# Kernel optimization log

Measured on AMD Instinct MI355X. Metric: run time of the kernel, lower is better.

## Reference

```python
import jax, jax.numpy as jnp
import numpy as np

N_NODES = 100000
N_EDGES = 1600000
D = 128  # h_feats


def setup_inputs() -> dict:
    key = jax.random.key(0)
    k1, k2, k3, k4 = jax.random.split(key, 4)
    x = jax.random.normal(k1, (N_NODES, D), dtype=jnp.float32)
    edge_index = jax.random.randint(k2, (2, N_EDGES), 0, N_NODES, dtype=jnp.int64)
    # Linear(2D -> D), torch layout [out, in]
    W1 = jax.random.normal(k3, (D, 2 * D), dtype=jnp.float32) * (1.0 / np.sqrt(2 * D))
    b1 = jnp.zeros((D,), dtype=jnp.float32)
    # Linear(D -> 1)
    W2 = jax.random.normal(k4, (1, D), dtype=jnp.float32) * (1.0 / np.sqrt(D))
    b2 = jnp.zeros((1,), dtype=jnp.float32)
    return {"x": x, "edge_index": edge_index, "W1": W1, "b1": b1, "W2": W2, "b2": b2}


def reference(x, edge_index, W1, b1, W2, b2):
    # gather both endpoints and concat along features: [E, 2D]
    h = jnp.concatenate([x[edge_index[0]], x[edge_index[1]]], axis=-1)
    h = jax.nn.relu(h @ W1.T + b1)          # [E, D]
    h = h @ W2.T + b2                        # [E, 1]
    return h.squeeze(1)                      # [E]
```

## Files before the change

### kernel.cpp

```cpp
#include <hip/hip_runtime.h>
#include <hip/hip_bf16.h>

#define N_NODES 100000
#define N_EDGES 1600000
#define NT32    3125
#define PRE_BLKS 625

#define BQ_OFF 12800000
#define SA_OFF 25600000
#define SB_OFF 26000000

typedef __attribute__((ext_vector_type(8))) short short8v;
typedef __attribute__((ext_vector_type(4))) float float4v;

__device__ __forceinline__ unsigned short f2bf(float f) {
    unsigned int u = __float_as_uint(f);
    u += 0x7fffu + ((u >> 16) & 1u);
    return (unsigned short)(u >> 16);
}
__device__ __forceinline__ unsigned int pack2bf(float a, float b) {
    return (unsigned int)f2bf(a) | ((unsigned int)f2bf(b) << 16);
}
__device__ __forceinline__ float2 bfpair(unsigned int w) {
    return float2{__uint_as_float(w << 16), __uint_as_float(w & 0xffff0000u)};
}
#define MAGICB 12583040.0f
__device__ __forceinline__ unsigned int qmagic(float f, float inv) {
    return __float_as_uint(fmaf(f, inv, MAGICB));
}

__device__ __forceinline__ void quant_store(
    const unsigned short* __restrict__ xlds, unsigned char* __restrict__ Q,
    float* __restrict__ S, int n0, int tid) {
    const int row = tid >> 3, part = tid & 7;
    const unsigned short* src = xlds + row * 132 + part * 16;
    uint4 w0 = *reinterpret_cast<const uint4*>(src);
    uint4 w1 = *reinterpret_cast<const uint4*>(src + 8);
    unsigned int ws[8] = {w0.x, w0.y, w0.z, w0.w, w1.x, w1.y, w1.z, w1.w};
    float m = 1e-6f;
#pragma unroll
    for (int k = 0; k < 8; ++k) {
        float2 f = bfpair(ws[k]);
        m = fmaxf(m, fmaxf(fabsf(f.x), fabsf(f.y)));
    }
    m = fmaxf(m, __shfl_xor(m, 1));
    m = fmaxf(m, __shfl_xor(m, 2));
    m = fmaxf(m, __shfl_xor(m, 4));
    const float inv = 127.0f / m;
    unsigned int ob[4];
#pragma unroll
    for (int k = 0; k < 4; ++k) {
        float2 f0 = bfpair(ws[2 * k]);
        float2 f1 = bfpair(ws[2 * k + 1]);
        unsigned int q0 = qmagic(f0.x, inv), q1 = qmagic(f0.y, inv);
        unsigned int q2 = qmagic(f1.x, inv), q3 = qmagic(f1.y, inv);
        ob[k] = (q0 & 0xffu) | ((q1 & 0xffu) << 8) |
                ((q2 & 0xffu) << 16) | (q3 << 24);
    }
    const int n = n0 + row;
    *reinterpret_cast<uint4*>(Q + (size_t)n * 128 + part * 16) =
        uint4{ob[0], ob[1], ob[2], ob[3]};
    if (part == 0) S[n] = m * (1.0f / 127.0f);
}

__global__ __launch_bounds__(256) void precompute_kernel(
    const float* __restrict__ x, const float* __restrict__ W1,
    const float* __restrict__ b1, unsigned char* __restrict__ Aq,
    unsigned char* __restrict__ Bq, float* __restrict__ sA,
    float* __restrict__ sB) {
    __shared__ unsigned short wlds[256 * 132];
    __shared__ unsigned short xlds[32 * 132];

    const int tid = threadIdx.x;
    const int wave = tid >> 6, lane = tid & 63;
    const int quad = lane >> 4, l15 = lane & 15;

    float4 b1v[4];
    if (wave < 2) {
#pragma unroll
        for (int j = 0; j < 4; ++j)
            b1v[j] = *reinterpret_cast<const float4*>(b1 + wave * 64 + j * 16 + quad * 4);
    }

#pragma unroll
    for (int i = 0; i < 32; ++i) {
        int fi = tid + i * 256;
        int jc = fi >> 5, c4 = fi & 31;
        float4 w4 = reinterpret_cast<const float4*>(
            W1)[(size_t)(jc & 127) * 64 + (jc >> 7) * 32 + c4];
        unsigned int* d = reinterpret_cast<unsigned int*>(&wlds[jc * 132 + c4 * 4]);
        d[0] = pack2bf(w4.x, w4.y);
        d[1] = pack2bf(w4.z, w4.w);
    }

    float4 xr[4];
    int t = blockIdx.x;
#pragma unroll
    for (int i = 0; i < 4; ++i) {
        int fi = tid + i * 256;
        int n = fi >> 5, c4 = fi & 31;
        xr[i] = reinterpret_cast<const float4*>(x)[(size_t)(t * 32 + n) * 32 + c4];
    }

    for (; t < NT32; t += PRE_BLKS) {
        __syncthreads();
#pragma unroll
        for (int i = 0; i < 4; ++i) {
            int fi = tid + i * 256;
            int n = fi >> 5, c4 = fi & 31;
            unsigned int* d = reinterpret_cast<unsigned int*>(&xlds[n * 132 + c4 * 4]);
            d[0] = pack2bf(xr[i].x, xr[i].y);
            d[1] = pack2bf(xr[i].z, xr[i].w);
        }
        __syncthreads();

        const int tn = t + PRE_BLKS;
        if (tn < NT32) {
#pragma unroll
            for (int i = 0; i < 4; ++i) {
                int fi = tid + i * 256;
                int n = fi >> 5, c4 = fi & 31;
                xr[i] = reinterpret_cast<const float4*>(x)[(size_t)(tn * 32 + n) * 32 + c4];
            }
        }

        float4v acc[2][4];
#pragma unroll
        for (int i = 0; i < 2; ++i)
#pragma unroll
            for (int j = 0; j < 4; ++j) acc[i][j] = float4v{0.f, 0.f, 0.f, 0.f};

#pragma unroll
        for (int s = 0; s < 4; ++s) {
            const int k0 = s * 32 + quad * 8;
            short8v xf[2], wf[4];
#pragma unroll
            for (int i = 0; i < 2; ++i)
                xf[i] = *reinterpret_cast<const short8v*>(&xlds[(i * 16 + l15) * 132 + k0]);
#pragma unroll
            for (int j = 0; j < 4; ++j)
                wf[j] = *reinterpret_cast<const short8v*>(
                    &wlds[(wave * 64 + j * 16 + l15) * 132 + k0]);
#pragma unroll
            for (int i = 0; i < 2; ++i)
#pragma unroll
                for (int j = 0; j < 4; ++j)
                    acc[i][j] = __builtin_amdgcn_mfma_f32_16x16x32_bf16(wf[j], xf[i], acc[i][j], 0, 0, 0);
        }
        __syncthreads();

        if (wave < 2) {
#pragma unroll
            for (int i = 0; i < 2; ++i)
#pragma unroll
                for (int j = 0; j < 4; ++j) {
                    const int col = wave * 64 + j * 16 + quad * 4;
                    float r0 = acc[i][j][0] + b1v[j].x;
                    float r1 = acc[i][j][1] + b1v[j].y;
                    float r2 = acc[i][j][2] + b1v[j].z;
                    float r3 = acc[i][j][3] + b1v[j].w;
                    uint2 st = {pack2bf(r0, r1), pack2bf(r2, r3)};
                    *reinterpret_cast<uint2*>(&xlds[(i * 16 + l15) * 132 + col]) = st;
                }
        }
        __syncthreads();
        quant_store(xlds, Aq, sA, t * 32, tid);
        __syncthreads();

        if (wave >= 2) {
#pragma unroll
            for (int i = 0; i < 2; ++i)
#pragma unroll
                for (int j = 0; j < 4; ++j) {
                    const int col = (wave - 2) * 64 + j * 16 + quad * 4;
                    uint2 st = {pack2bf(acc[i][j][0], acc[i][j][1]),
                                pack2bf(acc[i][j][2], acc[i][j][3])};
                    *reinterpret_cast<uint2*>(&xlds[(i * 16 + l15) * 132 + col]) = st;
                }
        }
        __syncthreads();
        quant_store(xlds, Bq, sB, t * 32, tid);
    }
}

template <bool IS64>
__device__ __forceinline__ void edge_loop(
    const long long* __restrict__ ei, const unsigned char* __restrict__ Aq,
    const unsigned char* __restrict__ Bq, const float* __restrict__ sA,
    const float* __restrict__ sB, const float* __restrict__ W2, float bias2,
    float* __restrict__ out, int wid, int nwaves, int eg, int sl) {
    const int k0 = sl * 32;
    float w2f[32];
#pragma unroll
    for (int j = 0; j < 8; ++j)
        *reinterpret_cast<float4*>(&w2f[j * 4]) =
            *reinterpret_cast<const float4*>(W2 + k0 + j * 4);
    const int* e32 = reinterpret_cast<const int*>(ei);

    for (int base = wid * 16; base < N_EDGES; base += nwaves * 16) {
        const int e = base + eg;
        int u, v;
        if (IS64) { u = (int)ei[e]; v = (int)ei[N_EDGES + e]; }
        else      { u = e32[e];     v = e32[N_EDGES + e]; }

        const uint4* pa = reinterpret_cast<const uint4*>(Aq + (unsigned)u * 128 + k0);
        const uint4* pb = reinterpret_cast<const uint4*>(Bq + (unsigned)v * 128 + k0);
        uint4 a0 = pa[0], a1 = pa[1];
        uint4 b0 = pb[0], b1w = pb[1];
        const float su = sA[u];
        const float sv = sB[v];
        const float r = sv * __builtin_amdgcn_rcpf(su);
        const float c = fmaf(r, 128.0f, 128.0f);

        unsigned int aw[8] = {a0.x, a0.y, a0.z, a0.w, a1.x, a1.y, a1.z, a1.w};
        unsigned int bw[8] = {b0.x, b0.y, b0.z, b0.w, b1w.x, b1w.y, b1w.z, b1w.w};

        float p = 0.f;
#pragma unroll
        for (int wi = 0; wi < 8; ++wi) {
#pragma unroll
            for (int byt = 0; byt < 4; ++byt) {
                float fa = (float)((aw[wi] >> (8 * byt)) & 0xffu);
                float fb = (float)((bw[wi] >> (8 * byt)) & 0xffu);
                float s = fmaxf(fmaf(fb, r, fa) - c, 0.f);
                p = fmaf(s, w2f[wi * 4 + byt], p);
            }
        }
        p += __shfl_xor(p, 1);
        p += __shfl_xor(p, 2);
        if (sl == 0) out[e] = fmaf(su, p, bias2);
    }
}

__global__ __launch_bounds__(256, 4) void edge_kernel(
    const long long* __restrict__ ei, const unsigned char* __restrict__ Aq,
    const unsigned char* __restrict__ Bq, const float* __restrict__ sA,
    const float* __restrict__ sB, const float* __restrict__ W2,
    const float* __restrict__ b2, float* __restrict__ out) {
    const int lane = threadIdx.x & 63;
    const int eg = lane >> 2;
    const int sl = lane & 3;
    const float bias2 = b2[0];

    const unsigned int hi = reinterpret_cast<const unsigned int*>(ei)[2 * lane + 1];
    const bool is64 = (__ballot(hi != 0) == 0ull);

    const int wid = (int)(((unsigned)(blockIdx.x * blockDim.x + threadIdx.x)) >> 6);
    const int nwaves = (int)(((unsigned)(gridDim.x * blockDim.x)) >> 6);

    if (is64) edge_loop<true>(ei, Aq, Bq, sA, sB, W2, bias2, out, wid, nwaves, eg, sl);
    else      edge_loop<false>(ei, Aq, Bq, sA, sB, W2, bias2, out, wid, nwaves, eg, sl);
}

extern "C" void kernel_launch(void* const* d_in, const int* in_sizes, int n_in,
                              void* d_out, int out_size, void* d_ws, size_t ws_size,
                              hipStream_t stream) {
    const float* x = (const float*)d_in[0];
    const long long* ei = (const long long*)d_in[1];
    const float* W1 = (const float*)d_in[2];
    const float* b1 = (const float*)d_in[3];
    const float* W2 = (const float*)d_in[4];
    const float* b2 = (const float*)d_in[5];
    float* out = (float*)d_out;

    unsigned char* Aq = (unsigned char*)d_ws;
    unsigned char* Bq = (unsigned char*)d_ws + BQ_OFF;
    float* sA = (float*)((char*)d_ws + SA_OFF);
    float* sB = (float*)((char*)d_ws + SB_OFF);

    precompute_kernel<<<PRE_BLKS, 256, 0, stream>>>(x, W1, b1, Aq, Bq, sA, sB);
    edge_kernel<<<2048, 256, 0, stream>>>(ei, Aq, Bq, sA, sB, W2, b2, out);
}
```

Before: 183.8 us.

## Keep W1 fragments in registers and quantize directly from MFMA accumulators

The precompute kernel no longer stages W1 in a large LDS buffer. Each wave loads its bf16 W1 fragments into registers once. Quantization now works straight on the accumulator values: per-row max is reduced with shuffles plus a small cross-wave LDS exchange, and the int8 bytes are packed into a small LDS buffer for coalesced stores to Aq and Bq. This cuts LDS usage so more blocks fit (launch bounds now ask for 3 per CU) and removes several syncs and bf16 round trips, at the cost of higher register pressure from holding 16 fragment vectors per thread. Scales are now computed from fp32 rather than bf16-rounded values, so the quantized output can differ slightly.

```diff
diff --git a/kernel.cpp b/kernel.cpp
--- a/kernel.cpp
+++ b/kernel.cpp
@@ -21,76 +21,48 @@
 __device__ __forceinline__ unsigned int pack2bf(float a, float b) {
     return (unsigned int)f2bf(a) | ((unsigned int)f2bf(b) << 16);
 }
-__device__ __forceinline__ float2 bfpair(unsigned int w) {
-    return float2{__uint_as_float(w << 16), __uint_as_float(w & 0xffff0000u)};
+__device__ __forceinline__ short8v pack8rne(float4 a, float4 b) {
+    union { unsigned int w[4]; short8v s; } u;
+    u.w[0] = pack2bf(a.x, a.y); u.w[1] = pack2bf(a.z, a.w);
+    u.w[2] = pack2bf(b.x, b.y); u.w[3] = pack2bf(b.z, b.w);
+    return u.s;
 }
 #define MAGICB 12583040.0f
 __device__ __forceinline__ unsigned int qmagic(float f, float inv) {
     return __float_as_uint(fmaf(f, inv, MAGICB));
 }
 
-__device__ __forceinline__ void quant_store(
-    const unsigned short* __restrict__ xlds, unsigned char* __restrict__ Q,
-    float* __restrict__ S, int n0, int tid) {
-    const int row = tid >> 3, part = tid & 7;
-    const unsigned short* src = xlds + row * 132 + part * 16;
-    uint4 w0 = *reinterpret_cast<const uint4*>(src);
-    uint4 w1 = *reinterpret_cast<const uint4*>(src + 8);
-    unsigned int ws[8] = {w0.x, w0.y, w0.z, w0.w, w1.x, w1.y, w1.z, w1.w};
-    float m = 1e-6f;
-#pragma unroll
-    for (int k = 0; k < 8; ++k) {
-        float2 f = bfpair(ws[k]);
-        m = fmaxf(m, fmaxf(fabsf(f.x), fabsf(f.y)));
-    }
-    m = fmaxf(m, __shfl_xor(m, 1));
-    m = fmaxf(m, __shfl_xor(m, 2));
-    m = fmaxf(m, __shfl_xor(m, 4));
-    const float inv = 127.0f / m;
-    unsigned int ob[4];
-#pragma unroll
-    for (int k = 0; k < 4; ++k) {
-        float2 f0 = bfpair(ws[2 * k]);
-        float2 f1 = bfpair(ws[2 * k + 1]);
-        unsigned int q0 = qmagic(f0.x, inv), q1 = qmagic(f0.y, inv);
-        unsigned int q2 = qmagic(f1.x, inv), q3 = qmagic(f1.y, inv);
-        ob[k] = (q0 & 0xffu) | ((q1 & 0xffu) << 8) |
-                ((q2 & 0xffu) << 16) | (q3 << 24);
-    }
-    const int n = n0 + row;
-    *reinterpret_cast<uint4*>(Q + (size_t)n * 128 + part * 16) =
-        uint4{ob[0], ob[1], ob[2], ob[3]};
-    if (part == 0) S[n] = m * (1.0f / 127.0f);
-}
-
-__global__ __launch_bounds__(256) void precompute_kernel(
+__global__ __launch_bounds__(256, 3) void precompute_kernel(
     const float* __restrict__ x, const float* __restrict__ W1,
     const float* __restrict__ b1, unsigned char* __restrict__ Aq,
     unsigned char* __restrict__ Bq, float* __restrict__ sA,
     float* __restrict__ sB) {
-    __shared__ unsigned short wlds[256 * 132];
     __shared__ unsigned short xlds[32 * 132];
+    __shared__ unsigned int bytebuf[32 * 68];
+    __shared__ float wmax[4][32];
 
     const int tid = threadIdx.x;
     const int wave = tid >> 6, lane = tid & 63;
     const int quad = lane >> 4, l15 = lane & 15;
 
+    const int jcb = wave * 64;
+    const int wrow = jcb & 127;
+    const int khalf = (jcb >> 7) * 128;
+    short8v wf[4][4];
+#pragma unroll
+    for (int j = 0; j < 4; ++j)
+#pragma unroll
+        for (int s = 0; s < 4; ++s) {
+            const float4* p = reinterpret_cast<const float4*>(
+                W1 + (size_t)(wrow + j * 16 + l15) * 256 + khalf + s * 32 + quad * 8);
+            wf[j][s] = pack8rne(p[0], p[1]);
+        }
+
     float4 b1v[4];
     if (wave < 2) {
 #pragma unroll
         for (int j = 0; j < 4; ++j)
-            b1v[j] = *reinterpret_cast<const float4*>(b1 + wave * 64 + j * 16 + quad * 4);
-    }
-
-#pragma unroll
-    for (int i = 0; i < 32; ++i) {
-        int fi = tid + i * 256;
-        int jc = fi >> 5, c4 = fi & 31;
-        float4 w4 = reinterpret_cast<const float4*>(
-            W1)[(size_t)(jc & 127) * 64 + (jc >> 7) * 32 + c4];
-        unsigned int* d = reinterpret_cast<unsigned int*>(&wlds[jc * 132 + c4 * 4]);
-        d[0] = pack2bf(w4.x, w4.y);
-        d[1] = pack2bf(w4.z, w4.w);
+            b1v[j] = *reinterpret_cast<const float4*>(b1 + jcb + j * 16 + quad * 4);
     }
 
     float4 xr[4];
@@ -133,53 +105,77 @@
 #pragma unroll
         for (int s = 0; s < 4; ++s) {
             const int k0 = s * 32 + quad * 8;
-            short8v xf[2], wf[4];
+            short8v xf[2];
 #pragma unroll
             for (int i = 0; i < 2; ++i)
                 xf[i] = *reinterpret_cast<const short8v*>(&xlds[(i * 16 + l15) * 132 + k0]);
 #pragma unroll
+            for (int i = 0; i < 2; ++i)
+#pragma unroll
+                for (int j = 0; j < 4; ++j)
+                    acc[i][j] = __builtin_amdgcn_mfma_f32_16x16x32_bf16(wf[j][s], xf[i], acc[i][j], 0, 0, 0);
+        }
+
+        if (wave < 2) {
+#pragma unroll
+            for (int i = 0; i < 2; ++i)
+#pragma unroll
+                for (int j = 0; j < 4; ++j) {
+                    acc[i][j][0] += b1v[j].x; acc[i][j][1] += b1v[j].y;
+                    acc[i][j][2] += b1v[j].z; acc[i][j][3] += b1v[j].w;
+                }
+        }
+        float m[2];
+#pragma unroll
+        for (int i = 0; i < 2; ++i) {
+            m[i] = 1e-6f;
+#pragma unroll
             for (int j = 0; j < 4; ++j)
-                wf[j] = *reinterpret_cast<const short8v*>(
-                    &wlds[(wave * 64 + j * 16 + l15) * 132 + k0]);
-#pragma unroll
-            for (int i = 0; i < 2; ++i)
-#pragma unroll
-                for (int j = 0; j < 4; ++j)
-                    acc[i][j] = __builtin_amdgcn_mfma_f32_16x16x32_bf16(wf[j], xf[i], acc[i][j], 0, 0, 0);
-        }
-        __syncthreads();
-
-        if (wave < 2) {
-#pragma unroll
-            for (int i = 0; i < 2; ++i)
-#pragma unroll
-                for (int j = 0; j < 4; ++j) {
-                    const int col = wave * 64 + j * 16 + quad * 4;
-                    float r0 = acc[i][j][0] + b1v[j].x;
-                    float r1 = acc[i][j][1] + b1v[j].y;
-                    float r2 = acc[i][j][2] + b1v[j].z;
-                    float r3 = acc[i][j][3] + b1v[j].w;
-                    uint2 st = {pack2bf(r0, r1), pack2bf(r2, r3)};
-                    *reinterpret_cast<uint2*>(&xlds[(i * 16 + l15) * 132 + col]) = st;
-                }
-        }
-        __syncthreads();
-        quant_store(xlds, Aq, sA, t * 32, tid);
-        __syncthreads();
-
-        if (wave >= 2) {
-#pragma unroll
-            for (int i = 0; i < 2; ++i)
-#pragma unroll
-                for (int j = 0; j < 4; ++j) {
-                    const int col = (wave - 2) * 64 + j * 16 + quad * 4;
-                    uint2 st = {pack2bf(acc[i][j][0], acc[i][j][1]),
-                                pack2bf(acc[i][j][2], acc[i][j][3])};
-                    *reinterpret_cast<uint2*>(&xlds[(i * 16 + l15) * 132 + col]) = st;
-                }
-        }
-        __syncthreads();
-        quant_store(xlds, Bq, sB, t * 32, tid);
+#pragma unroll
+                for (int r = 0; r < 4; ++r)
+                    m[i] = fmaxf(m[i], fabsf(acc[i][j][r]));
+            m[i] = fmaxf(m[i], __shfl_xor(m[i], 16));
+            m[i] = fmaxf(m[i], __shfl_xor(m[i], 32));
+        }
+        if (quad == 0) { wmax[wave][l15] = m[0]; wmax[wave][16 + l15] = m[1]; }
+        __syncthreads();
+
+        float inv[2];
+#pragma unroll
+        for (int i = 0; i < 2; ++i) {
+            float mh = fmaxf(m[i], wmax[wave ^ 1][i * 16 + l15]);
+            inv[i] = 127.0f / mh;
+            if (quad == 0 && (wave == 0 || wave == 2)) {
+                float* S = (wave == 0) ? sA : sB;
+                S[t * 32 + i * 16 + l15] = mh * (1.0f / 127.0f);
+            }
+        }
+
+#pragma unroll
+        for (int i = 0; i < 2; ++i)
+#pragma unroll
+            for (int j = 0; j < 4; ++j) {
+                unsigned int q0 = qmagic(acc[i][j][0], inv[i]);
+                unsigned int q1 = qmagic(acc[i][j][1], inv[i]);
+                unsigned int q2 = qmagic(acc[i][j][2], inv[i]);
+                unsigned int q3 = qmagic(acc[i][j][3], inv[i]);
+                unsigned int pk = (q0 & 0xffu) | ((q1 & 0xffu) << 8) |
+                                  ((q2 & 0xffu) << 16) | (q3 << 24);
+                bytebuf[(i * 16 + l15) * 68 + wave * 16 + j * 4 + quad] = pk;
+            }
+        __syncthreads();
+
+        {
+            const int row = tid >> 3, part = tid & 7;
+            const unsigned int* src = &bytebuf[row * 68 + part * 8];
+            uint4 o0 = *reinterpret_cast<const uint4*>(src);
+            uint4 o1 = *reinterpret_cast<const uint4*>(src + 4);
+            const int n = t * 32 + row;
+            unsigned char* dst = (part < 4) ? Aq : Bq;
+            const int cb = (part & 3) * 32;
+            *reinterpret_cast<uint4*>(dst + (size_t)n * 128 + cb) = o0;
+            *reinterpret_cast<uint4*>(dst + (size_t)n * 128 + cb + 16) = o1;
+        }
     }
 }
 
```

Result: faster. 179.1 us (-2.6%).
